# Performance work log

Hardware: AMD Instinct MI355X
Metric: run time of the kernel (lower is better)

The kernel has to match this reference:

```python
import jax, jax.numpy as jnp
import numpy as np

N_NODES = 100000
N_EDGES = 1200000
IN_FEATS = 128
HIDDEN = 64
OUT_FEATS = 40


def setup_inputs() -> dict:
    key = jax.random.key(0)
    k1, k2, k3, k4, k5 = jax.random.split(key, 5)
    x = jax.random.normal(k1, (N_NODES, IN_FEATS), dtype=jnp.float32)
    edge_index = jax.random.randint(k2, (2, N_EDGES), 0, N_NODES, dtype=jnp.int64)
    W1 = jax.random.normal(k3, (IN_FEATS, HIDDEN), dtype=jnp.float32) * (1.0 / np.sqrt(IN_FEATS))
    b1 = jnp.zeros((HIDDEN,), dtype=jnp.float32)
    W2 = jax.random.normal(k4, (HIDDEN, HIDDEN), dtype=jnp.float32) * (1.0 / np.sqrt(HIDDEN))
    b2 = jnp.zeros((HIDDEN,), dtype=jnp.float32)
    Wc = jax.random.normal(k5, (HIDDEN, OUT_FEATS), dtype=jnp.float32) * (1.0 / np.sqrt(HIDDEN))
    bc = jnp.zeros((OUT_FEATS,), dtype=jnp.float32)
    return {"x": x, "edge_index": edge_index, "W1": W1, "b1": b1,
            "W2": W2, "b2": b2, "Wc": Wc, "bc": bc}


def _gcn_norm(edge_index, n_nodes):
    # add self-loops, then symmetric normalization deg^{-1/2}[src] * deg^{-1/2}[dst]
    loops = jnp.arange(n_nodes, dtype=edge_index.dtype)
    src = jnp.concatenate([edge_index[0], loops])
    dst = jnp.concatenate([edge_index[1], loops])
    ones = jnp.ones(src.shape[0], dtype=jnp.float32)
    deg = jax.ops.segment_sum(ones, dst, num_segments=n_nodes)  # in-degree incl. self-loop
    dinv = jnp.where(deg > 0, jax.lax.rsqrt(deg), 0.0)
    norm = dinv[src] * dinv[dst]  # [E+N]
    return src, dst, norm


def _gcn_conv(h, W, b, src, dst, norm, n_nodes):
    h = h @ W                          # [N, F_out] dense transform first (PyG GCNConv)
    msg = h[src] * norm[:, None]       # gather + normalize, [E+N, F_out]
    out = jax.ops.segment_sum(msg, dst, num_segments=n_nodes)  # scatter-add
    return out + b


def reference(x, edge_index, W1, b1, W2, b2, Wc, bc):
    n = x.shape[0]
    src, dst, norm = _gcn_norm(edge_index, n)
    # dropout is identity in eval mode
    h = jax.nn.relu(_gcn_conv(x, W1, b1, src, dst, norm, n))
    embedding = _gcn_conv(h, W2, b2, src, dst, norm, n)
    logits = embedding @ Wc + bc
    soft_label = jax.nn.softmax(logits, axis=1)
    hard_label = jnp.argmax(soft_label, axis=1)
    return (logits, embedding, soft_label, hard_label)
```

## Files before the change

kernel.cpp:

```cpp
#include <hip/hip_runtime.h>
#include <hip/hip_bf16.h>
#include <math.h>

typedef __hip_bfloat16 bf16;

__device__ __forceinline__ float loadf(const void* p, size_t i, bool f32m) {
    return f32m ? ((const float*)p)[i]
                : __bfloat162float(((const bf16*)p)[i]);
}
__device__ __forceinline__ void storef(void* p, size_t i, float v, bool f32m) {
    if (f32m) ((float*)p)[i] = v;
    else      ((bf16*)p)[i] = __float2bfloat16(v);
}
__device__ __forceinline__ int ldidx(const int* w, size_t e, bool e64, size_t E, int row) {
    return e64 ? w[2 * (row * E + e)] : w[row * E + e];
}

__global__ void k_detect(const void* x, const int* ei, float* flags) {
    int lane = threadIdx.x;
    const unsigned short* hx = (const unsigned short*)x;
    unsigned short u = hx[2 * lane];
    int ex = (u >> 7) & 0xFF;
    bool tame = (ex >= 117 && ex <= 136);
    unsigned long long mt = __ballot(tame);
    unsigned long long mz = __ballot(ei[2 * lane + 1] != 0);
    if (lane == 0) {
        flags[0] = (__popcll(mt) >= 48) ? 0.0f : 1.0f;
        flags[1] = (mz == 0ULL) ? 1.0f : 0.0f;
    }
}


__global__ void k_zero_small(int* __restrict__ p, int m) {
    int i = blockIdx.x * 256 + threadIdx.x;
    if (i < m) p[i] = 0;
}

#define SCB_EPT 16

__global__ __launch_bounds__(256) void k_bucket_hist(const int* __restrict__ ei,
                                                     const float* __restrict__ flags,
                                                     int* __restrict__ bcnt, int E, int NB) {
    __shared__ int lcnt[512];
    bool e64 = flags[1] > 0.5f;
    int tid = threadIdx.x;
    for (int i = tid; i < NB; i += 256) lcnt[i] = 0;
    __syncthreads();
    int base = blockIdx.x * 256 * SCB_EPT;
#pragma unroll
    for (int j = 0; j < SCB_EPT; ++j) {
        int e = base + j * 256 + tid;
        if (e < E) atomicAdd(&lcnt[ldidx(ei, e, e64, E, 1) >> 8], 1);
    }
    __syncthreads();
    for (int i = tid; i < NB; i += 256) {
        int c = lcnt[i];
        if (c) atomicAdd(&bcnt[i], c);
    }
}

__global__ __launch_bounds__(512) void k_scan_buckets(const int* __restrict__ bcnt,
                                                      int* __restrict__ bbase,
                                                      int* __restrict__ bcur, int NB) {
    __shared__ int sh[512];
    int tid = threadIdx.x;
    int v = (tid < NB) ? bcnt[tid] : 0;
    sh[tid] = v;
    __syncthreads();
    for (int off = 1; off < 512; off <<= 1) {
        int t = (tid >= off) ? sh[tid - off] : 0;
        __syncthreads();
        sh[tid] += t;
        __syncthreads();
    }
    if (tid < NB) {
        int ex = sh[tid] - v;
        bbase[tid] = ex;
        bcur[tid] = ex;
    }
    if (tid == 0) bbase[NB] = sh[511];
}

__global__ __launch_bounds__(256) void k_bucket_scatter(const int* __restrict__ ei,
                                                        const float* __restrict__ flags,
                                                        int* __restrict__ bcur,
                                                        int2* __restrict__ recs,
                                                        int E, int NB) {
    __shared__ int lcnt[512], lrank[512], lbase[512];
    bool e64 = flags[1] > 0.5f;
    int tid = threadIdx.x;
    for (int i = tid; i < NB; i += 256) { lcnt[i] = 0; lrank[i] = 0; }
    __syncthreads();
    int base = blockIdx.x * 256 * SCB_EPT;
    int s[SCB_EPT], d[SCB_EPT];
#pragma unroll
    for (int j = 0; j < SCB_EPT; ++j) {
        int e = base + j * 256 + tid;
        if (e < E) {
            s[j] = ldidx(ei, e, e64, E, 0);
            d[j] = ldidx(ei, e, e64, E, 1);
            atomicAdd(&lcnt[d[j] >> 8], 1);
        } else d[j] = -1;
    }
    __syncthreads();
    for (int i = tid; i < NB; i += 256) {
        int c = lcnt[i];
        lbase[i] = c ? atomicAdd(&bcur[i], c) : 0;
    }
    __syncthreads();
#pragma unroll
    for (int j = 0; j < SCB_EPT; ++j) {
        if (d[j] >= 0) {
            int b = d[j] >> 8;
            int r = atomicAdd(&lrank[b], 1);
            recs[lbase[b] + r] = make_int2(s[j], d[j]);
        }
    }
}

__global__ __launch_bounds__(256) void k_bucket_csr(const int2* __restrict__ recs,
                                                    const int* __restrict__ bbase,
                                                    int* __restrict__ rowptr,
                                                    float* __restrict__ dinv,
                                                    int* __restrict__ srcs,
                                                    int n, int E) {
    __shared__ int lcnt[256];
    __shared__ int lcur[256];
    int b = blockIdx.x, tid = threadIdx.x;
    int e0 = bbase[b], e1 = bbase[b + 1];
    lcnt[tid] = 0;
    __syncthreads();
    for (int i = e0 + tid; i < e1; i += 256)
        atomicAdd(&lcnt[recs[i].y & 255], 1);
    __syncthreads();
    int c = lcnt[tid];
    lcur[tid] = c;
    __syncthreads();
    for (int off = 1; off < 256; off <<= 1) {
        int t = (tid >= off) ? lcur[tid - off] : 0;
        __syncthreads();
        lcur[tid] += t;
        __syncthreads();
    }
    int rp = bbase[b] + lcur[tid] - c;
    int node = (b << 8) + tid;
    if (node < n) {
        rowptr[node] = rp;
        dinv[node] = rsqrtf((float)(c + 1));
    }
    lcur[tid] = rp;
    __syncthreads();
    for (int i = e0 + tid; i < e1; i += 256) {
        int2 r = recs[i];
        int pos = atomicAdd(&lcur[r.y & 255], 1);
        srcs[pos] = r.x;
    }
    if (b == 0 && tid == 0) rowptr[n] = E;
}

template <int K, bool XF32>
__global__ __launch_bounds__(256) void k_gemm3(const void* __restrict__ Xa,
                                               const void* __restrict__ Xb,
                                               const void* __restrict__ W,
                                               const float* __restrict__ flags,
                                               const float* __restrict__ rowscale,
                                               float* __restrict__ out, int n) {
    __shared__ float xs[64 * (K + 4)];
    __shared__ float wl[K * 68];
    bool f32m = flags[0] > 0.5f;
    const void* X = f32m ? Xa : Xb;
    bool xf32 = XF32 || f32m;
    int tid = threadIdx.x;
    int r0 = blockIdx.x * 64;

    if (f32m) {
        for (int i = tid * 4; i < K * 64; i += 1024) {
            int k = i >> 6, cc = i & 63;
            float4 v = *(const float4*)((const float*)W + i);
            *(float4*)&wl[k * 68 + cc] = v;
        }
    } else {
        for (int i = tid; i < K * 64; i += 256) {
            int k = i >> 6, cc = i & 63;
            wl[k * 68 + cc] = __bfloat162float(((const bf16*)W)[i]);
        }
    }
    if (xf32) {
        for (int i = tid * 4; i < 64 * K; i += 1024) {
            int row = i / K, k = i % K;
            float4 v = {0, 0, 0, 0};
            if (r0 + row < n) v = *(const float4*)((const float*)X + (size_t)(r0 + row) * K + k);
            *(float4*)&xs[row * (K + 4) + k] = v;
        }
    } else {
        for (int i = tid * 4; i < 64 * K; i += 1024) {
            int row = i / K, k = i % K;
            float4 v = {0, 0, 0, 0};
            if (r0 + row < n) {
                const bf16* p = (const bf16*)X + (size_t)(r0 + row) * K + k;
                v.x = __bfloat162float(p[0]); v.y = __bfloat162float(p[1]);
                v.z = __bfloat162float(p[2]); v.w = __bfloat162float(p[3]);
            }
            *(float4*)&xs[row * (K + 4) + k] = v;
        }
    }
    __syncthreads();

    int lane = tid & 63, wv = tid >> 6;
    int rg = lane >> 4, cg = lane & 15;
    int rbase = wv * 16 + rg * 4;
    int cbase = cg * 4;

    float acc[4][4];
#pragma unroll
    for (int r = 0; r < 4; ++r)
#pragma unroll
        for (int c = 0; c < 4; ++c) acc[r][c] = 0.0f;

#pragma unroll 2
    for (int k = 0; k < K; k += 4) {
        float4 xrv[4], wv4[4];
#pragma unroll
        for (int r = 0; r < 4; ++r)
            xrv[r] = *(const float4*)&xs[(rbase + r) * (K + 4) + k];
#pragma unroll
        for (int j = 0; j < 4; ++j)
            wv4[j] = *(const float4*)&wl[(k + j) * 68 + cbase];
#pragma unroll
        for (int r = 0; r < 4; ++r) {
            const float* xp = (const float*)&xrv[r];
#pragma unroll
            for (int j = 0; j < 4; ++j) {
                float xv = xp[j];
                acc[r][0] += xv * wv4[j].x;
                acc[r][1] += xv * wv4[j].y;
                acc[r][2] += xv * wv4[j].z;
                acc[r][3] += xv * wv4[j].w;
            }
        }
    }

#pragma unroll
    for (int r = 0; r < 4; ++r) {
        int row = r0 + rbase + r;
        if (row < n) {
            float sc = rowscale[row];
            float4 st = {acc[r][0] * sc, acc[r][1] * sc, acc[r][2] * sc, acc[r][3] * sc};
            *(float4*)&out[(size_t)row * 64 + cbase] = st;
        }
    }
}

template <int EP>
__global__ __launch_bounds__(256) void k_agg(const float* __restrict__ t,
                                             const float* __restrict__ dinv,
                                             const int* __restrict__ rowptr,
                                             const int* __restrict__ srcs,
                                             const void* __restrict__ bias,
                                             const float* __restrict__ flags,
                                             void* __restrict__ d_out, size_t emb_base,
                                             float* __restrict__ B_ws, int n) {
    bool f32m = flags[0] > 0.5f;
    int wid = (blockIdx.x * 256 + threadIdx.x) >> 6;
    int lane = threadIdx.x & 63;
    if (wid >= n) return;
    float dv = dinv[wid];
    float acc = t[(size_t)wid * 64 + lane];
    int e0 = rowptr[wid], e1 = rowptr[wid + 1];
    for (int base = e0; base < e1; base += 64) {
        int m = e1 - base; if (m > 64) m = 64;
        int idx = base + lane;
        int s_l = (idx < e1) ? srcs[idx] : 0;
        int j = 0;
        for (; j + 8 <= m; j += 8) {
            int s0 = __shfl(s_l, j + 0, 64), s1 = __shfl(s_l, j + 1, 64);
            int s2 = __shfl(s_l, j + 2, 64), s3 = __shfl(s_l, j + 3, 64);
            int s4 = __shfl(s_l, j + 4, 64), s5 = __shfl(s_l, j + 5, 64);
            int s6 = __shfl(s_l, j + 6, 64), s7 = __shfl(s_l, j + 7, 64);
            float v0 = t[(size_t)s0 * 64 + lane];
            float v1 = t[(size_t)s1 * 64 + lane];
            float v2 = t[(size_t)s2 * 64 + lane];
            float v3 = t[(size_t)s3 * 64 + lane];
            float v4 = t[(size_t)s4 * 64 + lane];
            float v5 = t[(size_t)s5 * 64 + lane];
            float v6 = t[(size_t)s6 * 64 + lane];
            float v7 = t[(size_t)s7 * 64 + lane];
            acc += ((v0 + v1) + (v2 + v3)) + ((v4 + v5) + (v6 + v7));
        }
        for (; j < m; ++j) {
            int s = __shfl(s_l, j, 64);
            acc += t[(size_t)s * 64 + lane];
        }
    }
    acc = acc * dv + loadf(bias, lane, f32m);
    size_t oi = (size_t)wid * 64 + lane;
    if (EP == 0) acc = fmaxf(acc, 0.0f);
    if (f32m) {
        ((float*)d_out)[emb_base + oi] = acc;
    } else {
        B_ws[oi] = acc;
        if (EP == 1) ((bf16*)d_out)[emb_base + oi] = __float2bfloat16(acc);
    }
}

__global__ __launch_bounds__(256) void k_classifier(const float* __restrict__ flags,
                                                    const void* __restrict__ Wc,
                                                    const void* __restrict__ bc,
                                                    void* __restrict__ out,
                                                    size_t emb_base, size_t soft_base,
                                                    size_t hard_base,
                                                    const float* __restrict__ B_ws,
                                                    int n) {
    __shared__ float wc[40 * 65];
    __shared__ float bcs[40];
    __shared__ float ebuf[4][64];
    bool f32m = flags[0] > 0.5f;
    const float* emb = f32m ? ((const float*)out + emb_base) : B_ws;
    int tid = threadIdx.x;
    for (int i = tid; i < 64 * 40; i += 256) {
        int k = i / 40, cc = i % 40;
        wc[cc * 65 + k] = loadf(Wc, i, f32m);
    }
    if (tid < 40) bcs[tid] = loadf(bc, tid, f32m);
    __syncthreads();
    int w = tid >> 6, lane = tid & 63;

    for (int it = 0; it < 8; ++it) {
        int node = blockIdx.x * 32 + it * 4 + w;
        if (node >= n) continue;
        ebuf[w][lane] = emb[(size_t)node * 64 + lane];
        int c = lane;
        float acc = -INFINITY;
        if (c < 40) {
            acc = bcs[c];
            const float* wp = &wc[c * 65];
#pragma unroll
            for (int k = 0; k < 64; ++k) acc += ebuf[w][k] * wp[k];
            storef(out, (size_t)node * 40 + c, acc, f32m);
        }
        float m = acc;
#pragma unroll
        for (int off = 32; off > 0; off >>= 1) m = fmaxf(m, __shfl_xor(m, off, 64));
        float ex = (c < 40) ? expf(acc - m) : 0.0f;
        float s = ex;
#pragma unroll
        for (int off = 32; off > 0; off >>= 1) s += __shfl_xor(s, off, 64);
        if (c < 40) storef(out, soft_base + (size_t)node * 40 + c, ex / s, f32m);
        float bv = acc;
        int bi = (c < 40) ? c : 1000;
#pragma unroll
        for (int off = 32; off > 0; off >>= 1) {
            float ov = __shfl_xor(bv, off, 64);
            int oi = __shfl_xor(bi, off, 64);
            if (ov > bv || (ov == bv && oi < bi)) { bv = ov; bi = oi; }
        }
        if (lane == 0) storef(out, hard_base + node, (float)bi, f32m);
    }
}

extern "C" void kernel_launch(void* const* d_in, const int* in_sizes, int n_in,
                              void* d_out, int out_size, void* d_ws, size_t ws_size,
                              hipStream_t stream) {
    const void* x  = d_in[0];
    const int*  ei = (const int*)d_in[1];
    const void* W1 = d_in[2];
    const void* b1 = d_in[3];
    const void* W2 = d_in[4];
    const void* b2 = d_in[5];
    const void* Wc = d_in[6];
    const void* bc = d_in[7];

    const int n = in_sizes[0] / 128;
    const int E = in_sizes[1] / 2;
    const int NB = (n + 255) / 256;

    float* ws    = (float*)d_ws;
    const size_t npad = (((size_t)n + 1023) / 1024) * 1024;
    const size_t Epad = (((size_t)E + 255) / 256) * 256;
    float* flags  = ws;
    int*   bcnt   = (int*)(ws + 256);
    int*   bbase  = (int*)(ws + 768);
    int*   bcur   = (int*)(ws + 1536);
    int*   rowptr = (int*)(ws + 2048);
    float* dinv   = (float*)(rowptr + npad);
    int*   srcs   = (int*)(dinv + npad);
    float* A      = (float*)(srcs + Epad);
    float* B_ws   = A + (size_t)n * 64;
    int2*  recs   = (int2*)B_ws;

    const size_t emb_base  = (size_t)n * 40;
    const size_t soft_base = (size_t)n * 104;
    const size_t hard_base = (size_t)n * 144;
    float* h1_f32m = (float*)d_out + emb_base;

    const int gS  = (E + 256 * SCB_EPT - 1) / (256 * SCB_EPT);
    const int gG  = (n + 63) / 64;
    const int gW  = (n + 3) / 4;
    const int gC  = (n + 31) / 32;

    k_detect<<<1, 64, 0, stream>>>(x, ei, flags);

    k_zero_small<<<2, 256, 0, stream>>>(bcnt, 512);
    k_bucket_hist<<<gS, 256, 0, stream>>>(ei, flags, bcnt, E, NB);
    k_scan_buckets<<<1, 512, 0, stream>>>(bcnt, bbase, bcur, NB);
    k_bucket_scatter<<<gS, 256, 0, stream>>>(ei, flags, bcur, recs, E, NB);
    k_bucket_csr<<<NB, 256, 0, stream>>>(recs, bbase, rowptr, dinv, srcs, n, E);

    k_gemm3<128, false><<<gG, 256, 0, stream>>>(x, x, W1, flags, dinv, A, n);
    k_agg<0><<<gW, 256, 0, stream>>>(A, dinv, rowptr, srcs, b1, flags,
                                     d_out, emb_base, B_ws, n);

    k_gemm3<64, true><<<gG, 256, 0, stream>>>(h1_f32m, B_ws, W2, flags, dinv, A, n);
    k_agg<1><<<gW, 256, 0, stream>>>(A, dinv, rowptr, srcs, b2, flags,
                                     d_out, emb_base, B_ws, n);

    k_classifier<<<gC, 256, 0, stream>>>(flags, Wc, bc, d_out,
                                         emb_base, soft_base, hard_base, B_ws, n);
}
```

Baseline: 390.7 us.

## Restructure classifier to one thread per node with register accumulators

The classifier kernel now assigns one node per thread instead of one node per wavefront. Each thread keeps 40 logits in registers, reads its embedding row as float4 and broadcasts weights from shared memory. Softmax, max and argmax are computed serially in registers instead of with cross-lane shuffles, and outputs are written as vector row stores. This removes the idle lanes (40 of 64 were active) and the shuffle reductions, at the cost of higher register pressure, per-thread strided global accesses and fewer blocks.

```diff
diff --git a/kernel.cpp b/kernel.cpp
--- a/kernel.cpp
+++ b/kernel.cpp
@@ -303,6 +303,27 @@
     }
 }
 
+
+__device__ __forceinline__ void store_row40(void* out, size_t base, const float* a, bool f32m) {
+    if (f32m) {
+        float4* p = (float4*)((float*)out + base);
+#pragma unroll
+        for (int q = 0; q < 10; ++q) {
+            float4 st = {a[q * 4 + 0], a[q * 4 + 1], a[q * 4 + 2], a[q * 4 + 3]};
+            p[q] = st;
+        }
+    } else {
+        __hip_bfloat162* p = (__hip_bfloat162*)((bf16*)out + base);
+#pragma unroll
+        for (int i = 0; i < 20; ++i) {
+            __hip_bfloat162 h;
+            h.x = __float2bfloat16(a[2 * i]);
+            h.y = __float2bfloat16(a[2 * i + 1]);
+            p[i] = h;
+        }
+    }
+}
+
 __global__ __launch_bounds__(256) void k_classifier(const float* __restrict__ flags,
                                                     const void* __restrict__ Wc,
                                                     const void* __restrict__ bc,
@@ -311,51 +332,81 @@
                                                     size_t hard_base,
                                                     const float* __restrict__ B_ws,
                                                     int n) {
-    __shared__ float wc[40 * 65];
-    __shared__ float bcs[40];
-    __shared__ float ebuf[4][64];
+    __shared__ __align__(16) float wcs[64 * 40];
+    __shared__ __align__(16) float bcs[40];
     bool f32m = flags[0] > 0.5f;
     const float* emb = f32m ? ((const float*)out + emb_base) : B_ws;
     int tid = threadIdx.x;
-    for (int i = tid; i < 64 * 40; i += 256) {
-        int k = i / 40, cc = i % 40;
-        wc[cc * 65 + k] = loadf(Wc, i, f32m);
+
+    if (f32m) {
+        for (int i = tid * 4; i < 64 * 40; i += 1024)
+            *(float4*)&wcs[i] = *(const float4*)((const float*)Wc + i);
+    } else {
+        for (int i = tid; i < 64 * 40; i += 256)
+            wcs[i] = __bfloat162float(((const bf16*)Wc)[i]);
     }
     if (tid < 40) bcs[tid] = loadf(bc, tid, f32m);
     __syncthreads();
-    int w = tid >> 6, lane = tid & 63;
-
-    for (int it = 0; it < 8; ++it) {
-        int node = blockIdx.x * 32 + it * 4 + w;
-        if (node >= n) continue;
-        ebuf[w][lane] = emb[(size_t)node * 64 + lane];
-        int c = lane;
-        float acc = -INFINITY;
-        if (c < 40) {
-            acc = bcs[c];
-            const float* wp = &wc[c * 65];
-#pragma unroll
-            for (int k = 0; k < 64; ++k) acc += ebuf[w][k] * wp[k];
-            storef(out, (size_t)node * 40 + c, acc, f32m);
-        }
-        float m = acc;
-#pragma unroll
-        for (int off = 32; off > 0; off >>= 1) m = fmaxf(m, __shfl_xor(m, off, 64));
-        float ex = (c < 40) ? expf(acc - m) : 0.0f;
-        float s = ex;
-#pragma unroll
-        for (int off = 32; off > 0; off >>= 1) s += __shfl_xor(s, off, 64);
-        if (c < 40) storef(out, soft_base + (size_t)node * 40 + c, ex / s, f32m);
-        float bv = acc;
-        int bi = (c < 40) ? c : 1000;
-#pragma unroll
-        for (int off = 32; off > 0; off >>= 1) {
-            float ov = __shfl_xor(bv, off, 64);
-            int oi = __shfl_xor(bi, off, 64);
-            if (ov > bv || (ov == bv && oi < bi)) { bv = ov; bi = oi; }
-        }
-        if (lane == 0) storef(out, hard_base + node, (float)bi, f32m);
-    }
+
+    int node = blockIdx.x * 256 + tid;
+    if (node >= n) return;
+
+    float acc[40];
+#pragma unroll
+    for (int q = 0; q < 10; ++q) {
+        float4 b4 = *(const float4*)&bcs[q * 4];
+        acc[q * 4 + 0] = b4.x; acc[q * 4 + 1] = b4.y;
+        acc[q * 4 + 2] = b4.z; acc[q * 4 + 3] = b4.w;
+    }
+
+    const float4* erow = (const float4*)(emb + (size_t)node * 64);
+#pragma unroll 2
+    for (int j = 0; j < 16; ++j) {
+        float4 e4 = erow[j];
+        float ev[4] = {e4.x, e4.y, e4.z, e4.w};
+#pragma unroll
+        for (int kk = 0; kk < 4; ++kk) {
+            float e = ev[kk];
+            const float4* wr = (const float4*)&wcs[(j * 4 + kk) * 40];
+#pragma unroll
+            for (int q = 0; q < 10; ++q) {
+                float4 w = wr[q];
+                acc[q * 4 + 0] = fmaf(e, w.x, acc[q * 4 + 0]);
+                acc[q * 4 + 1] = fmaf(e, w.y, acc[q * 4 + 1]);
+                acc[q * 4 + 2] = fmaf(e, w.z, acc[q * 4 + 2]);
+                acc[q * 4 + 3] = fmaf(e, w.w, acc[q * 4 + 3]);
+            }
+        }
+    }
+
+    store_row40(out, (size_t)node * 40, acc, f32m);
+
+    float m0 = acc[0], m1 = acc[1], m2 = acc[2], m3 = acc[3];
+#pragma unroll
+    for (int q = 1; q < 10; ++q) {
+        m0 = fmaxf(m0, acc[q * 4 + 0]); m1 = fmaxf(m1, acc[q * 4 + 1]);
+        m2 = fmaxf(m2, acc[q * 4 + 2]); m3 = fmaxf(m3, acc[q * 4 + 3]);
+    }
+    float m = fmaxf(fmaxf(m0, m1), fmaxf(m2, m3));
+
+    int bi = 63;
+#pragma unroll
+    for (int c = 0; c < 40; ++c)
+        if (acc[c] == m && c < bi) bi = c;
+
+    float s = 0.0f;
+#pragma unroll
+    for (int c = 0; c < 40; ++c) {
+        float e = expf(acc[c] - m);
+        acc[c] = e;
+        s += e;
+    }
+    float rs = 1.0f / s;
+#pragma unroll
+    for (int c = 0; c < 40; ++c) acc[c] *= rs;
+
+    store_row40(out, soft_base + (size_t)node * 40, acc, f32m);
+    storef(out, hard_base + node, (float)bi, f32m);
 }
 
 extern "C" void kernel_launch(void* const* d_in, const int* in_sizes, int n_in,
@@ -396,7 +447,7 @@
     const int gS  = (E + 256 * SCB_EPT - 1) / (256 * SCB_EPT);
     const int gG  = (n + 63) / 64;
     const int gW  = (n + 3) / 4;
-    const int gC  = (n + 31) / 32;
+    const int gC  = (n + 255) / 256;
 
     k_detect<<<1, 64, 0, stream>>>(x, ei, flags);
 
```

New measurement: 342.4 us. -12.4%, faster.
